# Kernel optimization log

Measured on AMD Instinct MI355X. Metric: run time of the kernel, lower is better.

## Reference

```python
import jax, jax.numpy as jnp
import numpy as np

B, N, NPOINT, NSAMPLE = 16, 4096, 1024, 32
RADIUS = 0.2
CHANNELS = [6, 64, 64, 128]
EPS = 1e-5


def farthest_point_sample(xyz, npoint):
    # xyz: [B,N,3] -> idx [B,npoint]; deterministic start at index 0
    b, n, _ = xyz.shape
    def step(carry, _):
        dist, far = carry
        centroid = jnp.take_along_axis(xyz, far[:, None, None], axis=1)  # [B,1,3]
        d = jnp.sum((xyz - centroid) ** 2, axis=-1)  # [B,N]
        dist = jnp.minimum(dist, d)
        return (dist, jnp.argmax(dist, axis=-1).astype(jnp.int32)), far
    init = (jnp.full((b, n), 1e10, dtype=xyz.dtype), jnp.zeros((b,), jnp.int32))
    _, cents = jax.lax.scan(step, init, None, length=npoint)
    return cents.T  # [B,npoint]


def query_ball_point(radius, nsample, xyz, new_xyz):
    # xyz [B,N,3], new_xyz [B,S,3] -> idx [B,S,nsample]
    b, n, _ = xyz.shape
    d2 = (jnp.sum(new_xyz ** 2, -1)[:, :, None]
          + jnp.sum(xyz ** 2, -1)[:, None, :]
          - 2.0 * jnp.einsum('bsc,bnc->bsn', new_xyz, xyz))  # [B,S,N]
    cand = jnp.where(d2 > radius * radius, n, jnp.arange(n, dtype=jnp.int32)[None, None, :])
    # smallest nsample candidate indices (== torch sort[:, :, :nsample])
    neg_top, _ = jax.lax.top_k(-cand, nsample)
    idx = -neg_top  # ascending smallest indices
    first = idx[:, :, 0:1]
    return jnp.where(idx == n, first, idx)


def gather_points(pts, idx):
    # pts [B,N,C], idx [B,S,K] -> [B,S,K,C]
    b, s, k = idx.shape
    flat = idx.reshape(b, s * k)
    out = jnp.take_along_axis(pts, flat[:, :, None], axis=1)
    return out.reshape(b, s, k, pts.shape[-1])


def _forward(xyz, points, params):
    fps_idx = farthest_point_sample(xyz, NPOINT)  # [B,S]
    new_xyz = jnp.take_along_axis(xyz, fps_idx[:, :, None], axis=1)  # [B,S,3]
    idx = query_ball_point(RADIUS, NSAMPLE, xyz, new_xyz)  # [B,S,K]
    grouped_xyz = gather_points(xyz, idx) - new_xyz[:, :, None, :]  # [B,S,K,3]
    grouped_pts = gather_points(points, idx)  # [B,S,K,D]
    x = jnp.concatenate([grouped_xyz, grouped_pts], axis=-1)  # [B,S,K,6]
    for (W, g, bta, m, v) in params:
        x = jnp.einsum('bskc,cd->bskd', x, W)
        x = (x - m) * (g * jax.lax.rsqrt(v + EPS)) + bta  # BN (inference stats)
        x = jax.nn.relu(x)
    feat = jnp.max(x, axis=2)  # [B,S,Cout]
    return new_xyz, feat


def setup_inputs() -> dict:
    key = jax.random.key(0)
    ks = jax.random.split(key, 16)
    xyz = jax.random.uniform(ks[0], (B, N, 3), dtype=jnp.float32)
    points = jax.random.normal(ks[1], (B, N, 3), dtype=jnp.float32)
    inp = {'xyz': xyz, 'points': points}
    ki = 2
    for li in range(3):
        cin, cout = CHANNELS[li], CHANNELS[li + 1]
        inp[f'W{li+1}'] = jax.random.normal(ks[ki], (cin, cout), dtype=jnp.float32) * (1.0 / np.sqrt(cin)); ki += 1
        inp[f'g{li+1}'] = jnp.ones((cout,), jnp.float32)
        inp[f'b{li+1}'] = jnp.zeros((cout,), jnp.float32)
        inp[f'm{li+1}'] = jax.random.normal(ks[ki], (cout,), dtype=jnp.float32) * 0.1; ki += 1
        inp[f'v{li+1}'] = jax.random.uniform(ks[ki], (cout,), dtype=jnp.float32, minval=0.5, maxval=1.5); ki += 1
    return inp


def reference(xyz, points, W1, g1, b1, m1, v1, W2, g2, b2, m2, v2, W3, g3, b3, m3, v3):
    params = [(W1, g1, b1, m1, v1), (W2, g2, b2, m2, v2), (W3, g3, b3, m3, v3)]
    return _forward(xyz, points, params)
```

## Files before the change

### kernel.cpp

```cpp
#include <hip/hip_runtime.h>

#define BATCH   16
#define NPTS    4096
#define NPOINT  1024
#define NSAMPLE 32

typedef float v2f __attribute__((ext_vector_type(2)));

__global__ __attribute__((amdgpu_waves_per_eu(1, 1))) __launch_bounds__(256)
void fps_kernel(const float* __restrict__ xyz, float* __restrict__ new_xyz)
{
#pragma clang fp contract(off)
    const int b    = blockIdx.x;
    const int t    = threadIdx.x;
    const int lane = t & 63;
    const int wv   = t >> 6;
    const float* xb = xyz + (size_t)b * NPTS * 3;

    __shared__ float sxyz4[NPTS * 4];
    __shared__ __align__(16) unsigned long long sCand[2][4];

    v2f px2[8], py2[8], pz2[8], dist2[8];
#pragma unroll
    for (int j = 0; j < 16; ++j) {
        const int n = j * 256 + t;
        float X = xb[n * 3 + 0];
        float Y = xb[n * 3 + 1];
        float Z = xb[n * 3 + 2];
        sxyz4[n * 4 + 0] = X; sxyz4[n * 4 + 1] = Y; sxyz4[n * 4 + 2] = Z;
        asm volatile("" : "+v"(X), "+v"(Y), "+v"(Z));
        const int p = j >> 1;
        if (j & 1) { px2[p].y = X; py2[p].y = Y; pz2[p].y = Z; dist2[p].y = 1e10f; }
        else       { px2[p].x = X; py2[p].x = Y; pz2[p].x = Z; dist2[p].x = 1e10f; }
    }
    __syncthreads();

    float cx = sxyz4[0], cy = sxyz4[1], cz = sxyz4[2];
    float* out = new_xyz + (size_t)b * NPOINT * 3;

    for (int i = 0; i < NPOINT; ++i) {
        if (t == 0) { out[i*3+0] = cx; out[i*3+1] = cy; out[i*3+2] = cz; }

        v2f c2x; c2x.x = cx; c2x.y = cx;
        v2f c2y; c2y.x = cy; c2y.y = cy;
        v2f c2z; c2z.x = cz; c2z.y = cz;
#pragma unroll
        for (int p = 0; p < 8; ++p) {
            v2f dx = px2[p] - c2x;
            v2f dy = py2[p] - c2y;
            v2f dz = pz2[p] - c2z;
            v2f xx = dx * dx;
            v2f yy = dy * dy;
            v2f zz = dz * dz;
            v2f ss = (xx + yy) + zz;
            dist2[p].x = fminf(dist2[p].x, ss.x);
            dist2[p].y = fminf(dist2[p].y, ss.y);
        }

#define D(j) ((j) & 1 ? dist2[(j) >> 1].y : dist2[(j) >> 1].x)
        float mA = fmaxf(fmaxf(D(0),  D(1)),  D(2));
        float mB = fmaxf(fmaxf(D(3),  D(4)),  D(5));
        float mC = fmaxf(fmaxf(D(6),  D(7)),  D(8));
        float mD = fmaxf(fmaxf(D(9),  D(10)), D(11));
        float mE = fmaxf(fmaxf(D(12), D(13)), D(14));
        float mx = fmaxf(fmaxf(fmaxf(mA, mB), mC),
                         fmaxf(fmaxf(mD, mE), D(15)));
        int bj = 15;
#pragma unroll
        for (int j = 15; j >= 0; --j) bj = (D(j) == mx) ? j : bj;
#undef D
        const int bidx = bj * 256 + t;

        unsigned long long cand =
            ((unsigned long long)__float_as_uint(mx) << 32) |
            (unsigned long long)(unsigned int)~bidx;

#define DPP_RED(CTRL, RMASK)                                                   \
        {                                                                      \
            unsigned int oh = (unsigned int)__builtin_amdgcn_update_dpp(       \
                0, (int)(unsigned int)(cand >> 32), (CTRL), (RMASK), 0xF, true);\
            unsigned int ol = (unsigned int)__builtin_amdgcn_update_dpp(       \
                0, (int)(unsigned int)cand, (CTRL), (RMASK), 0xF, true);       \
            unsigned long long o =                                             \
                ((unsigned long long)oh << 32) | (unsigned long long)ol;       \
            if (o > cand) cand = o;                                            \
        }
        DPP_RED(0x121, 0xF)
        DPP_RED(0x122, 0xF)
        DPP_RED(0x124, 0xF)
        DPP_RED(0x128, 0xF)
        DPP_RED(0x142, 0xA)
        DPP_RED(0x143, 0xC)
#undef DPP_RED

        const int par = i & 1;
        if (lane == 63) sCand[par][wv] = cand;
        __syncthreads();

        const ulonglong2* pc = (const ulonglong2*)&sCand[par][0];
        ulonglong2 r0 = pc[0], r1 = pc[1];
        const float4* sx4 = (const float4*)sxyz4;
        float4 f0 = sx4[~(unsigned int)r0.x];
        float4 f1 = sx4[~(unsigned int)r0.y];
        float4 f2 = sx4[~(unsigned int)r1.x];
        float4 f3 = sx4[~(unsigned int)r1.y];
        bool s01 = r0.y > r0.x;
        bool s23 = r1.y > r1.x;
        unsigned long long m01 = s01 ? r0.y : r0.x;
        unsigned long long m23 = s23 ? r1.y : r1.x;
        float4 g01; g01.x = s01 ? f1.x : f0.x; g01.y = s01 ? f1.y : f0.y; g01.z = s01 ? f1.z : f0.z;
        float4 g23; g23.x = s23 ? f3.x : f2.x; g23.y = s23 ? f3.y : f2.y; g23.z = s23 ? f3.z : f2.z;
        bool sF = m23 > m01;
        cx = sF ? g23.x : g01.x;
        cy = sF ? g23.y : g01.y;
        cz = sF ? g23.z : g01.z;
    }
}

__global__ __launch_bounds__(256)
void ball_kernel(const float* __restrict__ xyz, const float* __restrict__ new_xyz,
                 int* __restrict__ idx)
{
    const int q    = blockIdx.x * 4 + (threadIdx.x >> 6);
    const int lane = threadIdx.x & 63;
    const int b    = q >> 10;
    const float* xb = xyz + (size_t)b * NPTS * 3;

    const float s0 = new_xyz[q*3+0];
    const float s1 = new_xyz[q*3+1];
    const float s2 = new_xyz[q*3+2];
    const float ssum = __fadd_rn(__fadd_rn(__fmul_rn(s0,s0), __fmul_rn(s1,s1)),
                                 __fmul_rn(s2,s2));
    const float r2 = (float)(0.2 * 0.2);

    int* myidx = idx + (size_t)q * NSAMPLE;
    int found = 0;
    int first = -1;

    for (int c = 0; c < NPTS / 64 && found < NSAMPLE; ++c) {
        int n = c * 64 + lane;
        float x = xb[n*3+0], y = xb[n*3+1], z = xb[n*3+2];
        float nsum = __fadd_rn(__fadd_rn(__fmul_rn(x,x), __fmul_rn(y,y)), __fmul_rn(z,z));
        float dot  = __fmaf_rn(s2, z, __fmaf_rn(s1, y, __fmul_rn(s0, x)));
        float d2   = __fsub_rn(__fadd_rn(ssum, nsum), __fmul_rn(2.0f, dot));
        bool inb = !(d2 > r2);
        unsigned long long m = __ballot(inb);
        if (first < 0 && m != 0ull) first = c * 64 + (int)__builtin_ctzll(m);
        if (inb) {
            int rank = __popcll(m & ((1ull << lane) - 1ull));
            int slot = found + rank;
            if (slot < NSAMPLE) myidx[slot] = n;
        }
        found += __popcll(m);
    }
    if (found > NSAMPLE) found = NSAMPLE;
    for (int slot = found + lane; slot < NSAMPLE; slot += 64) myidx[slot] = first;
}

__global__ __launch_bounds__(256)
void mlp_kernel(const float* __restrict__ xyz, const float* __restrict__ points,
                const float* __restrict__ new_xyz, const int* __restrict__ idx,
                const float* __restrict__ W1, const float* __restrict__ g1,
                const float* __restrict__ b1, const float* __restrict__ m1,
                const float* __restrict__ v1,
                const float* __restrict__ W2, const float* __restrict__ g2,
                const float* __restrict__ b2, const float* __restrict__ m2,
                const float* __restrict__ v2,
                const float* __restrict__ W3, const float* __restrict__ g3,
                const float* __restrict__ b3, const float* __restrict__ m3,
                const float* __restrict__ v3,
                float* __restrict__ feat)
{
    __shared__ float w1t[64][8];
    __shared__ float w2t[64][64];
    __shared__ float w3t[128][64];
    __shared__ float bias1s[64], bias2s[64], bias3s[128];
    __shared__ float sc1[64], sc2[64], sc3[128];

    const int tid = threadIdx.x;

    for (int d = tid; d < 64; d += 256) {
        float s1v = g1[d] / sqrtf(v1[d] + 1e-5f);
        sc1[d] = s1v; bias1s[d] = b1[d] - m1[d] * s1v;
        float s2v = g2[d] / sqrtf(v2[d] + 1e-5f);
        sc2[d] = s2v; bias2s[d] = b2[d] - m2[d] * s2v;
    }
    for (int d = tid; d < 128; d += 256) {
        float s3v = g3[d] / sqrtf(v3[d] + 1e-5f);
        sc3[d] = s3v; bias3s[d] = b3[d] - m3[d] * s3v;
    }
    __syncthreads();
    for (int e = tid; e < 64 * 8; e += 256) {
        int d = e >> 3, c = e & 7;
        w1t[d][c] = (c < 6) ? W1[c * 64 + d] * sc1[d] : 0.f;
    }
    for (int e = tid; e < 64 * 64; e += 256) {
        int d = e >> 6, c = e & 63;
        w2t[d][c] = W2[c * 64 + d] * sc2[d];
    }
    for (int e = tid; e < 128 * 64; e += 256) {
        int d = e >> 6, c = e & 63;
        w3t[d][c] = W3[c * 128 + d] * sc3[d];
    }
    __syncthreads();

    const int wid  = tid >> 6;
    const int lane = tid & 63;
    const int q = blockIdx.x * 8 + wid * 2 + (lane >> 5);
    const int k = lane & 31;
    const int b = q >> 10;

    const int n = idx[(size_t)q * NSAMPLE + k];
    const float* xp = xyz    + ((size_t)b * NPTS + n) * 3;
    const float* pp = points + ((size_t)b * NPTS + n) * 3;
    const float* nx = new_xyz + (size_t)q * 3;

    const float in0 = __fsub_rn(xp[0], nx[0]);
    const float in1 = __fsub_rn(xp[1], nx[1]);
    const float in2 = __fsub_rn(xp[2], nx[2]);
    const float in3 = pp[0], in4 = pp[1], in5 = pp[2];

    float x1[64];
#pragma unroll
    for (int d = 0; d < 64; ++d) {
        const float4 wa = *(const float4*)&w1t[d][0];
        const float4 wb = *(const float4*)&w1t[d][4];
        float acc = bias1s[d];
        acc = fmaf(in0, wa.x, acc);
        acc = fmaf(in1, wa.y, acc);
        acc = fmaf(in2, wa.z, acc);
        acc = fmaf(in3, wa.w, acc);
        acc = fmaf(in4, wb.x, acc);
        acc = fmaf(in5, wb.y, acc);
        x1[d] = fmaxf(acc, 0.f);
    }

    float x2[64];
#pragma unroll
    for (int d = 0; d < 64; ++d) {
        float acc = bias2s[d];
        const float4* wr = (const float4*)w2t[d];
#pragma unroll
        for (int cc = 0; cc < 16; ++cc) {
            float4 w = wr[cc];
            acc = fmaf(x1[4*cc+0], w.x, acc);
            acc = fmaf(x1[4*cc+1], w.y, acc);
            acc = fmaf(x1[4*cc+2], w.z, acc);
            acc = fmaf(x1[4*cc+3], w.w, acc);
        }
        x2[d] = fmaxf(acc, 0.f);
    }

    float* fq = feat + (size_t)q * 128;
    for (int d = 0; d < 128; ++d) {
        float acc = bias3s[d];
        const float4* wr = (const float4*)w3t[d];
#pragma unroll
        for (int cc = 0; cc < 16; ++cc) {
            float4 w = wr[cc];
            acc = fmaf(x2[4*cc+0], w.x, acc);
            acc = fmaf(x2[4*cc+1], w.y, acc);
            acc = fmaf(x2[4*cc+2], w.z, acc);
            acc = fmaf(x2[4*cc+3], w.w, acc);
        }
        float vv = fmaxf(acc, 0.f);
#pragma unroll
        for (int off = 16; off >= 1; off >>= 1)
            vv = fmaxf(vv, __shfl_xor(vv, off));
        if (k == 0) fq[d] = vv;
    }
}

extern "C" void kernel_launch(void* const* d_in, const int* in_sizes, int n_in,
                              void* d_out, int out_size, void* d_ws, size_t ws_size,
                              hipStream_t stream)
{
    (void)in_sizes; (void)n_in; (void)out_size; (void)ws_size;

    const float* xyz    = (const float*)d_in[0];
    const float* points = (const float*)d_in[1];
    const float* W1 = (const float*)d_in[2];
    const float* g1 = (const float*)d_in[3];
    const float* b1 = (const float*)d_in[4];
    const float* m1 = (const float*)d_in[5];
    const float* v1 = (const float*)d_in[6];
    const float* W2 = (const float*)d_in[7];
    const float* g2 = (const float*)d_in[8];
    const float* b2 = (const float*)d_in[9];
    const float* m2 = (const float*)d_in[10];
    const float* v2 = (const float*)d_in[11];
    const float* W3 = (const float*)d_in[12];
    const float* g3 = (const float*)d_in[13];
    const float* b3 = (const float*)d_in[14];
    const float* m3 = (const float*)d_in[15];
    const float* v3 = (const float*)d_in[16];

    float* out_f    = (float*)d_out;
    float* new_xyz  = out_f;
    float* feat     = out_f + (size_t)BATCH * NPOINT * 3;
    int*   idx      = (int*)d_ws;

    fps_kernel <<<BATCH, 256, 0, stream>>>(xyz, new_xyz);
    ball_kernel<<<(BATCH * NPOINT) / 4, 256, 0, stream>>>(xyz, new_xyz, idx);
    mlp_kernel <<<(BATCH * NPOINT) / 8, 256, 0, stream>>>(xyz, points, new_xyz, idx,
        W1, g1, b1, m1, v1, W2, g2, b2, m2, v2, W3, g3, b3, m3, v3, feat);
}
```

Before: 953.9 us.

## Stream MLP weights from global memory with output-stationary register accumulators

The MLP kernel no longer stages transposed, scale-folded weights in shared memory. Each layer now uses a 64-wide register accumulator and loops over input channels, reading weight rows directly from global memory as wave-uniform float4 loads, then applies the BN scale and bias afterwards. Layer 3 runs in two halves of 64 outputs, with vectorised float4 stores, and the kernel is pinned to 2 waves per EU. This removes the per-block weight transpose and LDS traffic, in exchange for cache-dependent global loads and higher register pressure.

```diff
diff --git a/kernel.cpp b/kernel.cpp
--- a/kernel.cpp
+++ b/kernel.cpp
@@ -157,7 +157,7 @@
     for (int slot = found + lane; slot < NSAMPLE; slot += 64) myidx[slot] = first;
 }
 
-__global__ __launch_bounds__(256)
+__global__ __attribute__((amdgpu_waves_per_eu(2, 2))) __launch_bounds__(256)
 void mlp_kernel(const float* __restrict__ xyz, const float* __restrict__ points,
                 const float* __restrict__ new_xyz, const int* __restrict__ idx,
                 const float* __restrict__ W1, const float* __restrict__ g1,
@@ -171,36 +171,18 @@
                 const float* __restrict__ v3,
                 float* __restrict__ feat)
 {
-    __shared__ float w1t[64][8];
-    __shared__ float w2t[64][64];
-    __shared__ float w3t[128][64];
-    __shared__ float bias1s[64], bias2s[64], bias3s[128];
-    __shared__ float sc1[64], sc2[64], sc3[128];
+    __shared__ float sc1[64], bi1[64], sc2[64], bi2[64], sc3[128], bi3[128];
 
     const int tid = threadIdx.x;
-
     for (int d = tid; d < 64; d += 256) {
         float s1v = g1[d] / sqrtf(v1[d] + 1e-5f);
-        sc1[d] = s1v; bias1s[d] = b1[d] - m1[d] * s1v;
+        sc1[d] = s1v; bi1[d] = b1[d] - m1[d] * s1v;
         float s2v = g2[d] / sqrtf(v2[d] + 1e-5f);
-        sc2[d] = s2v; bias2s[d] = b2[d] - m2[d] * s2v;
+        sc2[d] = s2v; bi2[d] = b2[d] - m2[d] * s2v;
     }
     for (int d = tid; d < 128; d += 256) {
         float s3v = g3[d] / sqrtf(v3[d] + 1e-5f);
-        sc3[d] = s3v; bias3s[d] = b3[d] - m3[d] * s3v;
-    }
-    __syncthreads();
-    for (int e = tid; e < 64 * 8; e += 256) {
-        int d = e >> 3, c = e & 7;
-        w1t[d][c] = (c < 6) ? W1[c * 64 + d] * sc1[d] : 0.f;
-    }
-    for (int e = tid; e < 64 * 64; e += 256) {
-        int d = e >> 6, c = e & 63;
-        w2t[d][c] = W2[c * 64 + d] * sc2[d];
-    }
-    for (int e = tid; e < 128 * 64; e += 256) {
-        int d = e >> 6, c = e & 63;
-        w3t[d][c] = W3[c * 128 + d] * sc3[d];
+        sc3[d] = s3v; bi3[d] = b3[d] - m3[d] * s3v;
     }
     __syncthreads();
 
@@ -215,59 +197,89 @@
     const float* pp = points + ((size_t)b * NPTS + n) * 3;
     const float* nx = new_xyz + (size_t)q * 3;
 
-    const float in0 = __fsub_rn(xp[0], nx[0]);
-    const float in1 = __fsub_rn(xp[1], nx[1]);
-    const float in2 = __fsub_rn(xp[2], nx[2]);
-    const float in3 = pp[0], in4 = pp[1], in5 = pp[2];
-
-    float x1[64];
-#pragma unroll
-    for (int d = 0; d < 64; ++d) {
-        const float4 wa = *(const float4*)&w1t[d][0];
-        const float4 wb = *(const float4*)&w1t[d][4];
-        float acc = bias1s[d];
-        acc = fmaf(in0, wa.x, acc);
-        acc = fmaf(in1, wa.y, acc);
-        acc = fmaf(in2, wa.z, acc);
-        acc = fmaf(in3, wa.w, acc);
-        acc = fmaf(in4, wb.x, acc);
-        acc = fmaf(in5, wb.y, acc);
-        x1[d] = fmaxf(acc, 0.f);
-    }
-
-    float x2[64];
-#pragma unroll
-    for (int d = 0; d < 64; ++d) {
-        float acc = bias2s[d];
-        const float4* wr = (const float4*)w2t[d];
-#pragma unroll
-        for (int cc = 0; cc < 16; ++cc) {
-            float4 w = wr[cc];
-            acc = fmaf(x1[4*cc+0], w.x, acc);
-            acc = fmaf(x1[4*cc+1], w.y, acc);
-            acc = fmaf(x1[4*cc+2], w.z, acc);
-            acc = fmaf(x1[4*cc+3], w.w, acc);
-        }
-        x2[d] = fmaxf(acc, 0.f);
-    }
+    float in[6];
+    in[0] = __fsub_rn(xp[0], nx[0]);
+    in[1] = __fsub_rn(xp[1], nx[1]);
+    in[2] = __fsub_rn(xp[2], nx[2]);
+    in[3] = pp[0]; in[4] = pp[1]; in[5] = pp[2];
+
+    float x[64];
+    float acc[64];
+
+#pragma unroll
+    for (int d = 0; d < 64; ++d) acc[d] = 0.f;
+#pragma unroll
+    for (int c = 0; c < 6; ++c) {
+        const float4* wr = (const float4*)(W1 + c * 64);
+        const float xc = in[c];
+#pragma unroll
+        for (int dd = 0; dd < 16; ++dd) {
+            float4 w = wr[dd];
+            acc[4*dd+0] = fmaf(xc, w.x, acc[4*dd+0]);
+            acc[4*dd+1] = fmaf(xc, w.y, acc[4*dd+1]);
+            acc[4*dd+2] = fmaf(xc, w.z, acc[4*dd+2]);
+            acc[4*dd+3] = fmaf(xc, w.w, acc[4*dd+3]);
+        }
+    }
+#pragma unroll
+    for (int d = 0; d < 64; ++d)
+        x[d] = fmaxf(fmaf(acc[d], sc1[d], bi1[d]), 0.f);
+
+#pragma unroll
+    for (int d = 0; d < 64; ++d) acc[d] = 0.f;
+#pragma unroll
+    for (int c = 0; c < 64; ++c) {
+        const float4* wr = (const float4*)(W2 + c * 64);
+        const float xc = x[c];
+#pragma unroll
+        for (int dd = 0; dd < 16; ++dd) {
+            float4 w = wr[dd];
+            acc[4*dd+0] = fmaf(xc, w.x, acc[4*dd+0]);
+            acc[4*dd+1] = fmaf(xc, w.y, acc[4*dd+1]);
+            acc[4*dd+2] = fmaf(xc, w.z, acc[4*dd+2]);
+            acc[4*dd+3] = fmaf(xc, w.w, acc[4*dd+3]);
+        }
+    }
+#pragma unroll
+    for (int d = 0; d < 64; ++d)
+        x[d] = fmaxf(fmaf(acc[d], sc2[d], bi2[d]), 0.f);
 
     float* fq = feat + (size_t)q * 128;
-    for (int d = 0; d < 128; ++d) {
-        float acc = bias3s[d];
-        const float4* wr = (const float4*)w3t[d];
-#pragma unroll
-        for (int cc = 0; cc < 16; ++cc) {
-            float4 w = wr[cc];
-            acc = fmaf(x2[4*cc+0], w.x, acc);
-            acc = fmaf(x2[4*cc+1], w.y, acc);
-            acc = fmaf(x2[4*cc+2], w.z, acc);
-            acc = fmaf(x2[4*cc+3], w.w, acc);
-        }
-        float vv = fmaxf(acc, 0.f);
-#pragma unroll
-        for (int off = 16; off >= 1; off >>= 1)
-            vv = fmaxf(vv, __shfl_xor(vv, off));
-        if (k == 0) fq[d] = vv;
+#pragma unroll
+    for (int half = 0; half < 2; ++half) {
+#pragma unroll
+        for (int d = 0; d < 64; ++d) acc[d] = 0.f;
+#pragma unroll
+        for (int c = 0; c < 64; ++c) {
+            const float4* wr = (const float4*)(W3 + c * 128 + half * 64);
+            const float xc = x[c];
+#pragma unroll
+            for (int dd = 0; dd < 16; ++dd) {
+                float4 w = wr[dd];
+                acc[4*dd+0] = fmaf(xc, w.x, acc[4*dd+0]);
+                acc[4*dd+1] = fmaf(xc, w.y, acc[4*dd+1]);
+                acc[4*dd+2] = fmaf(xc, w.z, acc[4*dd+2]);
+                acc[4*dd+3] = fmaf(xc, w.w, acc[4*dd+3]);
+            }
+        }
+#pragma unroll
+        for (int dg = 0; dg < 16; ++dg) {
+            float st[4];
+#pragma unroll
+            for (int j = 0; j < 4; ++j) {
+                const int d = dg * 4 + j;
+                const int dc = half * 64 + d;
+                float vv = fmaxf(fmaf(acc[d], sc3[dc], bi3[dc]), 0.f);
+#pragma unroll
+                for (int off = 16; off >= 1; off >>= 1)
+                    vv = fmaxf(vv, __shfl_xor(vv, off));
+                st[j] = vv;
+            }
+            if (k == 0) {
+                float4 v4; v4.x = st[0]; v4.y = st[1]; v4.z = st[2]; v4.w = st[3];
+                *(float4*)&fq[half * 64 + dg * 4] = v4;
+            }
+        }
     }
 }
 
```

Result: slower. 1.636 ms (+71.6%).
